# Optimization experiments

Hardware: AMD Instinct MI355X
Metric: run time of the kernel (lower is better)

The kernel has to match this reference:

```python
import jax, jax.numpy as jnp
import numpy as np

M_CH = 3        # channel index from shapelet_info['pos'][1]
DIL = 4         # dilation
EPS = 1e-8      # pDic['scale_epsilon']


def setup_inputs() -> dict:
    key = jax.random.key(0)
    k1, k2 = jax.random.split(key, 2)
    B, C, Q, L = 512, 8, 4096, 32
    W = Q - (L - 1) * DIL  # 3972
    x = jax.random.normal(k1, (B, C, Q), dtype=jnp.float32)
    shapelet = jax.random.normal(k2, (L,), dtype=jnp.float32)
    posMap = jnp.zeros((W,), dtype=jnp.float32)
    posSlope = jnp.float32(1.0)
    return {"x": x, "shapelet": shapelet, "posMap": posMap, "posSlope": posSlope, "ep": 1}


def reference(x, shapelet, posMap, posSlope, ep):
    # x: [B, C, Q]; pick channel m, dilated unfold -> [B, W, L]
    B, C, Q = x.shape
    L = shapelet.shape[0]
    W = Q - (L - 1) * DIL
    xc = x[:, M_CH, :]                                        # [B, Q]
    idx = jnp.arange(W)[:, None] + jnp.arange(L)[None, :] * DIL  # [W, L]
    xu = xc[:, idx]                                           # [B, W, L]
    # scaleType == 2: z-normalize each subsequence (torch.std is unbiased -> ddof=1)
    mean = jnp.mean(xu, axis=-1, keepdims=True)
    std = jnp.std(xu, axis=-1, ddof=1, keepdims=True)
    xu = (xu - mean) / (std + EPS)
    # squared distance, mean over L
    d = jnp.mean((shapelet[None, None, :] - xu) ** 2, axis=-1)  # [B, W]
    # positional weighting: posSlope*elu(-posMap) + 2.0
    w = posSlope * jax.nn.elu(-posMap) + 2.0                  # [W]
    ftrs = d * w[None, :]                                     # [B, W] (sum over singleton channel dim is identity)
    agg = jnp.min(ftrs, axis=-1)                              # [B]
    return jax.nn.relu(agg)[:, None]                          # [B, 1]
```

## Files before the change

kernel.cpp:

```cpp
#include <hip/hip_runtime.h>
#include <math.h>

#define EPSC 1e-8f
#define LC   32
#define QC   4096
#define WC   3972
#define NU   993
#define RUN  8

__device__ __forceinline__ int skew(int a) { return a + (a >> 6); }

__global__ __launch_bounds__(512, 4) void feature_kernel(
    const float* __restrict__ x,
    const float* __restrict__ shp,
    const float* __restrict__ posMap,
    const float* __restrict__ posSlope_p,
    float* __restrict__ out,
    int C)
{
    __shared__ float sx[4352];
    __shared__ float sw[4160];
    __shared__ float smin[8];

    const int tid = threadIdx.x;
    const int b   = blockIdx.x;
    const float* __restrict__ xr = x + ((size_t)b * C + 3) * QC;

    {
        const float4* xr4 = reinterpret_cast<const float4*>(xr);
        #pragma unroll
        for (int i = 0; i < 2; ++i) {
            int a4 = tid + i * 512;
            float4 v = xr4[a4];
            int s = skew(a4 * 4);
            sx[s] = v.x; sx[s+1] = v.y; sx[s+2] = v.z; sx[s+3] = v.w;
        }
    }
    {
        const float ps = posSlope_p[0];
        const float4* pm4 = reinterpret_cast<const float4*>(posMap);
        #pragma unroll
        for (int i = 0; i < 2; ++i) {
            int a4 = tid + i * 512;
            if (a4 < NU) {
                float4 z = pm4[a4];
                float e0 = (-z.x > 0.f) ? -z.x : (__expf(-z.x) - 1.f);
                float e1 = (-z.y > 0.f) ? -z.y : (__expf(-z.y) - 1.f);
                float e2 = (-z.z > 0.f) ? -z.z : (__expf(-z.z) - 1.f);
                float e3 = (-z.w > 0.f) ? -z.w : (__expf(-z.w) - 1.f);
                int s = skew(a4 * 4);
                sw[s]   = fmaf(ps, e0, 2.0f);
                sw[s+1] = fmaf(ps, e1, 2.0f);
                sw[s+2] = fmaf(ps, e2, 2.0f);
                sw[s+3] = fmaf(ps, e3, 2.0f);
            }
        }
    }
    __syncthreads();

    float sreg[LC];
    #pragma unroll
    for (int j = 0; j < LC; ++j) sreg[j] = shp[j];
    float Ssum = 0.f, S2 = 0.f;
    #pragma unroll
    for (int j = 0; j < LC; ++j) { Ssum += sreg[j]; S2 = fmaf(sreg[j], sreg[j], S2); }

    const int lane = tid & 63;
    const int wv_id = tid >> 6;
    const int r    = wv_id & 3;
    const int gl   = ((wv_id >> 2) << 6) | lane;
    const int u0   = gl * RUN;

    float buf[32];
    #pragma unroll
    for (int p = 0; p < 32; ++p)
        buf[p] = sx[skew(r + 4 * (u0 + p))];

    float a0=0,a1=0,a2=0,a3=0, q0=0,q1=0,q2=0,q3=0;
    #pragma unroll
    for (int p = 0; p < 32; p += 4) {
        a0 += buf[p];   q0 = fmaf(buf[p],   buf[p],   q0);
        a1 += buf[p+1]; q1 = fmaf(buf[p+1], buf[p+1], q1);
        a2 += buf[p+2]; q2 = fmaf(buf[p+2], buf[p+2], q2);
        a3 += buf[p+3]; q3 = fmaf(buf[p+3], buf[p+3], q3);
    }
    float sum = (a0+a1)+(a2+a3);
    float sq  = (q0+q1)+(q2+q3);

    const float invL  = 1.0f / 32.0f;
    const float invL1 = 1.0f / 31.0f;
    float best = INFINITY;

    #pragma unroll
    for (int k = 0; k < RUN; ++k) {
        if (k > 0) {
            int slot = (k + 31) & 31;
            float oldv = buf[slot];
            float newv = sx[skew(r + 4 * (u0 + k + 31))];
            sum += newv - oldv;
            sq  += fmaf(newv, newv, -(oldv * oldv));
            buf[slot] = newv;
        }
        float d0=0,d1=0,d2=0,d3=0;
        #pragma unroll
        for (int j = 0; j < LC; j += 4) {
            d0 = fmaf(sreg[j],   buf[(k+j)   & 31], d0);
            d1 = fmaf(sreg[j+1], buf[(k+j+1) & 31], d1);
            d2 = fmaf(sreg[j+2], buf[(k+j+2) & 31], d2);
            d3 = fmaf(sreg[j+3], buf[(k+j+3) & 31], d3);
        }
        float dot = (d0+d1)+(d2+d3);

        const int  u     = u0 + k;
        const bool valid = u < NU;
        float wvv = sw[skew(r + 4 * u)];

        float m   = sum * invL;
        float var = (sq - 32.0f * m * m) * invL1;
        var = fmaxf(var, 1e-30f);
        float inv = __builtin_amdgcn_rsqf(var);
        float d = S2 * invL
                - 2.0f * (dot - m * Ssum) * invL * inv
                + (sq * invL - m * m) * inv * inv;

        float f = valid ? d * wvv : INFINITY;
        best = fminf(best, f);
    }

    #pragma unroll
    for (int off = 32; off > 0; off >>= 1)
        best = fminf(best, __shfl_down(best, off, 64));
    if (lane == 0) smin[wv_id] = best;
    __syncthreads();
    if (tid == 0) {
        float m0 = fminf(fminf(smin[0], smin[1]), fminf(smin[2], smin[3]));
        float m1 = fminf(fminf(smin[4], smin[5]), fminf(smin[6], smin[7]));
        out[b] = fmaxf(fminf(m0, m1), 0.0f);
    }
}

extern "C" void kernel_launch(void* const* d_in, const int* in_sizes, int n_in,
                              void* d_out, int out_size, void* d_ws, size_t ws_size,
                              hipStream_t stream) {
    const float* x        = (const float*)d_in[0];
    const float* shp      = (const float*)d_in[1];
    const float* posMap   = (const float*)d_in[2];
    const float* posSlope = (const float*)d_in[3];
    float* out = (float*)d_out;

    const int C = 8;
    const int B = in_sizes[0] / (C * QC);

    feature_kernel<<<B, 512, 0, stream>>>(x, shp, posMap, posSlope, out, C);
}
```

Measured before the change: 11.50 us.

## Compute position weights in registers and simplify distance algebra

Drops the shared-memory table of position weights: each thread now loads its own posMap entries straight from global memory and evaluates the ELU weight in registers. This frees LDS and removes a staging pass, and the posMap loads can overlap the x staging. The distance formula is also rewritten so the (sq/L - m^2)*inv^2 term becomes the constant 31/32, leaving a single FMA per window. This assumes var*inv^2 == 1, which ignores EPS, and the variance floor changes from 1e-30 to 1e-24, so near-constant windows may be treated slightly differently.

```diff
diff --git a/kernel.cpp b/kernel.cpp
--- a/kernel.cpp
+++ b/kernel.cpp
@@ -1,12 +1,11 @@
 #include <hip/hip_runtime.h>
 #include <math.h>
 
-#define EPSC 1e-8f
-#define LC   32
-#define QC   4096
-#define WC   3972
-#define NU   993
-#define RUN  8
+#define LC  32
+#define QC  4096
+#define WC  3972
+#define NU  993
+#define RUN 8
 
 __device__ __forceinline__ int skew(int a) { return a + (a >> 6); }
 
@@ -19,15 +18,28 @@
     int C)
 {
     __shared__ float sx[4352];
-    __shared__ float sw[4160];
     __shared__ float smin[8];
 
-    const int tid = threadIdx.x;
-    const int b   = blockIdx.x;
-    const float* __restrict__ xr = x + ((size_t)b * C + 3) * QC;
+    const int tid   = threadIdx.x;
+    const int b     = blockIdx.x;
+    const int lane  = tid & 63;
+    const int wv_id = tid >> 6;
+    const int r     = wv_id & 3;
+    const int gl    = ((wv_id >> 2) << 6) | lane;
+    const int u0    = gl * RUN;
+    const int w0    = r + 4 * u0;
+
+    const float ps = posSlope_p[0];
+    float pwv[RUN];
+    #pragma unroll
+    for (int k = 0; k < RUN; ++k) {
+        int w  = w0 + 4 * k;
+        int wi = (w < WC) ? w : (WC - 1);
+        pwv[k] = posMap[wi];
+    }
 
     {
-        const float4* xr4 = reinterpret_cast<const float4*>(xr);
+        const float4* xr4 = reinterpret_cast<const float4*>(x + ((size_t)b * C + 3) * QC);
         #pragma unroll
         for (int i = 0; i < 2; ++i) {
             int a4 = tid + i * 512;
@@ -36,27 +48,13 @@
             sx[s] = v.x; sx[s+1] = v.y; sx[s+2] = v.z; sx[s+3] = v.w;
         }
     }
-    {
-        const float ps = posSlope_p[0];
-        const float4* pm4 = reinterpret_cast<const float4*>(posMap);
-        #pragma unroll
-        for (int i = 0; i < 2; ++i) {
-            int a4 = tid + i * 512;
-            if (a4 < NU) {
-                float4 z = pm4[a4];
-                float e0 = (-z.x > 0.f) ? -z.x : (__expf(-z.x) - 1.f);
-                float e1 = (-z.y > 0.f) ? -z.y : (__expf(-z.y) - 1.f);
-                float e2 = (-z.z > 0.f) ? -z.z : (__expf(-z.z) - 1.f);
-                float e3 = (-z.w > 0.f) ? -z.w : (__expf(-z.w) - 1.f);
-                int s = skew(a4 * 4);
-                sw[s]   = fmaf(ps, e0, 2.0f);
-                sw[s+1] = fmaf(ps, e1, 2.0f);
-                sw[s+2] = fmaf(ps, e2, 2.0f);
-                sw[s+3] = fmaf(ps, e3, 2.0f);
-            }
-        }
+
+    #pragma unroll
+    for (int k = 0; k < RUN; ++k) {
+        float z = -pwv[k];
+        float e = (z > 0.f) ? z : (__expf(z) - 1.f);
+        pwv[k] = fmaf(ps, e, 2.0f);
     }
-    __syncthreads();
 
     float sreg[LC];
     #pragma unroll
@@ -64,17 +62,14 @@
     float Ssum = 0.f, S2 = 0.f;
     #pragma unroll
     for (int j = 0; j < LC; ++j) { Ssum += sreg[j]; S2 = fmaf(sreg[j], sreg[j], S2); }
+    const float C0 = S2 * (1.0f / 32.0f) + 31.0f / 32.0f;
 
-    const int lane = tid & 63;
-    const int wv_id = tid >> 6;
-    const int r    = wv_id & 3;
-    const int gl   = ((wv_id >> 2) << 6) | lane;
-    const int u0   = gl * RUN;
+    __syncthreads();
 
     float buf[32];
     #pragma unroll
     for (int p = 0; p < 32; ++p)
-        buf[p] = sx[skew(r + 4 * (u0 + p))];
+        buf[p] = sx[skew(w0 + 4 * p)];
 
     float a0=0,a1=0,a2=0,a3=0, q0=0,q1=0,q2=0,q3=0;
     #pragma unroll
@@ -87,8 +82,6 @@
     float sum = (a0+a1)+(a2+a3);
     float sq  = (q0+q1)+(q2+q3);
 
-    const float invL  = 1.0f / 32.0f;
-    const float invL1 = 1.0f / 31.0f;
     float best = INFINITY;
 
     #pragma unroll
@@ -96,7 +89,7 @@
         if (k > 0) {
             int slot = (k + 31) & 31;
             float oldv = buf[slot];
-            float newv = sx[skew(r + 4 * (u0 + k + 31))];
+            float newv = sx[skew(w0 + 4 * (k + 31))];
             sum += newv - oldv;
             sq  += fmaf(newv, newv, -(oldv * oldv));
             buf[slot] = newv;
@@ -111,19 +104,13 @@
         }
         float dot = (d0+d1)+(d2+d3);
 
-        const int  u     = u0 + k;
-        const bool valid = u < NU;
-        float wvv = sw[skew(r + 4 * u)];
-
-        float m   = sum * invL;
-        float var = (sq - 32.0f * m * m) * invL1;
-        var = fmaxf(var, 1e-30f);
+        float m   = sum * (1.0f / 32.0f);
+        float var = (sq - 32.0f * m * m) * (1.0f / 31.0f);
+        var = fmaxf(var, 1e-24f);
         float inv = __builtin_amdgcn_rsqf(var);
-        float d = S2 * invL
-                - 2.0f * (dot - m * Ssum) * invL * inv
-                + (sq * invL - m * m) * inv * inv;
-
-        float f = valid ? d * wvv : INFINITY;
+        float t   = fmaf(-m, Ssum, dot);
+        float d   = fmaf(-t * (1.0f / 16.0f), inv, C0);
+        float f   = ((u0 + k) < NU) ? d * pwv[k] : INFINITY;
         best = fminf(best, f);
     }
 
```

Result: slower. 13.89 us, median of 2 (+20.8%).
